# Optimization experiments

Measured on AMD Instinct MI355X. Metric: run time of the kernel, lower is better.

## Reference

```python
import jax, jax.numpy as jnp
import numpy as np

DIM = 512
HEADS = 8
DIM_HEAD = 64
INNER = HEADS * DIM_HEAD
SCALE = DIM_HEAD ** -0.5


def setup_inputs() -> dict:
    key = jax.random.key(0)
    ks = jax.random.split(key, 6)
    b, n = 2, 2048
    x = jax.random.normal(ks[0], (b, n, DIM), dtype=jnp.float32)
    # torch Linear(dim, 3*inner, bias=False): store as [in, out] for x @ W
    w_qkv = jax.random.normal(ks[1], (DIM, 3 * INNER), dtype=jnp.float32) * (DIM ** -0.5)
    # Conv2d(heads, heads, 1, bias=False) weights squeezed to [out_h, in_h]
    w_pre = jax.random.normal(ks[2], (HEADS, HEADS), dtype=jnp.float32) * (HEADS ** -0.5)
    w_post = jax.random.normal(ks[3], (HEADS, HEADS), dtype=jnp.float32) * (HEADS ** -0.5)
    w_out = jax.random.normal(ks[4], (INNER, DIM), dtype=jnp.float32) * (INNER ** -0.5)
    b_out = jax.random.normal(ks[5], (DIM,), dtype=jnp.float32) * 0.01
    return {"x": x, "w_qkv": w_qkv, "w_pre": w_pre, "w_post": w_post,
            "w_out": w_out, "b_out": b_out}


def reference(x, w_qkv, w_pre, w_post, w_out, b_out):
    b, n, _ = x.shape
    qkv = x @ w_qkv  # [b, n, 3*inner]
    q, k, v = jnp.split(qkv, 3, axis=-1)
    # b n (h d) -> b h n d
    split_heads = lambda t: t.reshape(b, n, HEADS, DIM_HEAD).transpose(0, 2, 1, 3)
    q, k, v = split_heads(q), split_heads(k), split_heads(v)
    dots = jnp.einsum('bhid,bhjd->bhij', q, k) * SCALE
    # pre-softmax talking-heads: 1x1 conv over the head axis
    dots = jnp.einsum('gh,bhij->bgij', w_pre, dots)
    attn = jax.nn.softmax(dots, axis=-1)
    # post-softmax talking-heads mix
    attn = jnp.einsum('gh,bhij->bgij', w_post, attn)
    out = jnp.einsum('bhij,bhjd->bhid', attn, v)
    out = out.transpose(0, 2, 1, 3).reshape(b, n, INNER)  # b h n d -> b n (h d)
    return out @ w_out + b_out
```

## Files before the change

### kernel.cpp

```cpp
#include <hip/hip_runtime.h>
#include <hip/hip_bf16.h>

typedef unsigned short ushort_t;
typedef __attribute__((ext_vector_type(8))) short short8;
typedef __attribute__((ext_vector_type(4))) short short4v;
typedef __attribute__((ext_vector_type(4))) float floatx4;

#define MFMA16(a, b, c) __builtin_amdgcn_mfma_f32_16x16x32_bf16(a, b, c, 0, 0, 0)

__device__ __forceinline__ float bf2f(ushort_t u) {
    unsigned int v = ((unsigned int)u) << 16;
    return __int_as_float((int)v);
}
__device__ __forceinline__ ushort_t f2bf(float f) {
    unsigned int x = (unsigned int)__float_as_int(f);
    unsigned int r = (x + 0x7FFFu + ((x >> 16) & 1u)) >> 16;
    return (ushort_t)r;
}

__global__ __launch_bounds__(256) void k_cvt(const floatx4* __restrict__ src,
                                             short4v* __restrict__ dst, int n4) {
    int i = blockIdx.x * 256 + threadIdx.x;
    if (i < n4) {
        floatx4 v = src[i];
        short4v o;
        o[0] = (short)f2bf(v[0]);
        o[1] = (short)f2bf(v[1]);
        o[2] = (short)f2bf(v[2]);
        o[3] = (short)f2bf(v[3]);
        dst[i] = o;
    }
}

__global__ __launch_bounds__(256) void k_transpose_cvt(const float* __restrict__ src,
                                                       ushort_t* __restrict__ dst, int R, int C) {
    __shared__ float t[32][33];
    int tx = threadIdx.x & 31, ty = threadIdx.x >> 5;
    int r0 = blockIdx.y * 32, c0 = blockIdx.x * 32;
    for (int y = ty; y < 32; y += 8) t[y][tx] = src[(r0 + y) * C + c0 + tx];
    __syncthreads();
    for (int y = ty; y < 32; y += 8) dst[(c0 + y) * R + r0 + tx] = f2bf(t[tx][y]);
}

__global__ __launch_bounds__(256) void k_qkv(const ushort_t* __restrict__ x,
                                             const ushort_t* __restrict__ wt,
                                             ushort_t* __restrict__ qs,
                                             ushort_t* __restrict__ ks,
                                             ushort_t* __restrict__ vt) {
    __shared__ __align__(16) ushort_t st[64 * 72];
    const int tid = threadIdx.x, lane = tid & 63, wv = tid >> 6;
    const int col = lane & 15, quad = lane >> 4;
    const int row0 = blockIdx.y * 64 + (wv >> 1) * 32;
    const int c0 = blockIdx.x * 64 + (wv & 1) * 32;
    const int which = blockIdx.x >> 3, hh = blockIdx.x & 7;
    const int brow0 = blockIdx.y * 64;
    const int bb = brow0 >> 11, n0 = brow0 & 2047;
    const int hidx = bb * 8 + hh;
    floatx4 acc[2][2];
#pragma unroll
    for (int i = 0; i < 2; i++)
#pragma unroll
        for (int j = 0; j < 2; j++) acc[i][j] = (floatx4){0.f, 0.f, 0.f, 0.f};
    for (int k0 = 0; k0 < 512; k0 += 32) {
        const int ko = k0 + quad * 8;
        short8 a0 = *(const short8*)&x[(row0 + col) * 512 + ko];
        short8 a1 = *(const short8*)&x[(row0 + 16 + col) * 512 + ko];
        short8 b0 = *(const short8*)&wt[(c0 + col) * 512 + ko];
        short8 b1 = *(const short8*)&wt[(c0 + 16 + col) * 512 + ko];
        acc[0][0] = MFMA16(a0, b0, acc[0][0]);
        acc[0][1] = MFMA16(a0, b1, acc[0][1]);
        acc[1][0] = MFMA16(a1, b0, acc[1][0]);
        acc[1][1] = MFMA16(a1, b1, acc[1][1]);
    }
    const float qscale = (which == 0) ? 0.125f : 1.0f;
#pragma unroll
    for (int i = 0; i < 2; i++)
#pragma unroll
        for (int j = 0; j < 2; j++)
#pragma unroll
            for (int r = 0; r < 4; r++) {
                int il = (wv >> 1) * 32 + i * 16 + quad * 4 + r;
                int cl = (wv & 1) * 32 + j * 16 + col;
                ushort_t hv = f2bf(acc[i][j][r] * qscale);
                if (which == 2) st[cl * 72 + il] = hv;
                else            st[il * 72 + cl] = hv;
            }
    __syncthreads();
    if (which < 2) {
        ushort_t* dst = (which == 0) ? qs : ks;
#pragma unroll
        for (int s = tid; s < 512; s += 256) {
            int rr = s >> 3, dc = (s & 7) * 8;
            *(short8*)&dst[(hidx * 2048 + n0 + rr) * 64 + dc] = *(const short8*)&st[rr * 72 + dc];
        }
    } else {
#pragma unroll
        for (int s = tid; s < 512; s += 256) {
            int d = s >> 3, nc = (s & 7) * 8;
            *(short8*)&vt[(hidx * 64 + d) * 2048 + n0 + nc] = *(const short8*)&st[d * 72 + nc];
        }
    }
}

__global__ __launch_bounds__(512, 2) void k_attn(const ushort_t* __restrict__ qs,
                                                 const ushort_t* __restrict__ ks,
                                                 const ushort_t* __restrict__ vt,
                                                 const float* __restrict__ w_pre,
                                                 const float* __restrict__ w_post,
                                                 const ushort_t* __restrict__ wot,
                                                 const float* __restrict__ bias,
                                                 float* __restrict__ out) {
    __shared__ __align__(16) ushort_t qlds[8 * 16 * 72];
    __shared__ __align__(16) ushort_t U[8 * 16 * 136];
    __shared__ __align__(16) ushort_t oline[16 * 520];
    __shared__ float wbuf[128];
    __shared__ float lred[8][8][16];
    __shared__ float linv[8][16];
    const int tid = threadIdx.x, lane = tid & 63, wv = tid >> 6;
    const int col = lane & 15, quad = lane >> 4;
    const int b = blockIdx.y, n0 = blockIdx.x * 16;
    const int e = wv;

    if (tid < 64) wbuf[tid] = w_pre[tid];
    else if (tid < 128) wbuf[tid] = w_post[tid - 64];
    for (int c = tid; c < 1024; c += 512) {
        int hh = c >> 7, rem = c & 127, ii = rem >> 3, dc = (rem & 7) * 8;
        *(short8*)&qlds[(hh * 16 + ii) * 72 + dc] =
            *(const short8*)&qs[((b * 8 + hh) * 2048 + n0 + ii) * 64 + dc];
    }
    __syncthreads();

    float Lacc[8][4];
    floatx4 Oa[8][4];
#pragma unroll
    for (int g = 0; g < 8; g++) {
#pragma unroll
        for (int r = 0; r < 4; r++) Lacc[g][r] = 0.f;
#pragma unroll
        for (int nt = 0; nt < 4; nt++) Oa[g][nt] = (floatx4){0.f, 0.f, 0.f, 0.f};
    }

    for (int jt = 0; jt < 16; jt++) {
        const int j0 = jt * 128;
        const int jw = j0 + wv * 16;
        floatx4 S[8];
#pragma unroll
        for (int h = 0; h < 8; h++) {
            const ushort_t* qb = &qlds[(h * 16 + col) * 72 + quad * 8];
            short8 a0 = *(const short8*)&qb[0];
            short8 a1 = *(const short8*)&qb[32];
            const ushort_t* kb = &ks[((b * 8 + h) * 2048 + jw + col) * 64 + quad * 8];
            short8 b0 = *(const short8*)&kb[0];
            short8 b1 = *(const short8*)&kb[32];
            floatx4 a = (floatx4){0.f, 0.f, 0.f, 0.f};
            a = MFMA16(a0, b0, a);
            a = MFMA16(a1, b1, a);
            S[h] = a;
        }
#pragma unroll
        for (int g = 0; g < 8; g++)
#pragma unroll
            for (int r = 0; r < 4; r++) {
                float s = 0.f;
#pragma unroll
                for (int h = 0; h < 8; h++) s = fmaf(wbuf[g * 8 + h], S[h][r], s);
                float u = __expf(s);
                Lacc[g][r] += u;
                U[(g * 16 + quad * 4 + r) * 136 + wv * 16 + col] = f2bf(u);
            }
        __syncthreads();
#pragma unroll
        for (int k2 = 0; k2 < 4; k2++) {
            short8 bf[4];
#pragma unroll
            for (int nt = 0; nt < 4; nt++)
                bf[nt] = *(const short8*)&vt[((b * 8 + e) * 64 + nt * 16 + col) * 2048 + j0 +
                                             k2 * 32 + quad * 8];
            short8 af[8];
#pragma unroll
            for (int g = 0; g < 8; g++)
                af[g] = *(const short8*)&U[(g * 16 + col) * 136 + k2 * 32 + quad * 8];
#pragma unroll
            for (int g = 0; g < 8; g++)
#pragma unroll
                for (int nt = 0; nt < 4; nt++) Oa[g][nt] = MFMA16(af[g], bf[nt], Oa[g][nt]);
        }
        __syncthreads();
    }

#pragma unroll
    for (int g = 0; g < 8; g++)
#pragma unroll
        for (int r = 0; r < 4; r++) {
            float v = Lacc[g][r];
            v += __shfl_xor(v, 1, 64);
            v += __shfl_xor(v, 2, 64);
            v += __shfl_xor(v, 4, 64);
            v += __shfl_xor(v, 8, 64);
            if (col == 0) lred[wv][g][quad * 4 + r] = v;
        }
    __syncthreads();
    if (tid < 128) {
        int g = tid >> 4, ii = tid & 15;
        float l = 0.f;
#pragma unroll
        for (int w2 = 0; w2 < 8; w2++) l += lred[w2][g][ii];
        linv[g][ii] = 1.0f / l;
    }
    __syncthreads();
    float coef[8][4];
#pragma unroll
    for (int g = 0; g < 8; g++) {
        float wqe = wbuf[64 + e * 8 + g];
#pragma unroll
        for (int r = 0; r < 4; r++) coef[g][r] = wqe * linv[g][quad * 4 + r];
    }
#pragma unroll
    for (int nt = 0; nt < 4; nt++)
#pragma unroll
        for (int r = 0; r < 4; r++) {
            float o = 0.f;
#pragma unroll
            for (int g = 0; g < 8; g++) o = fmaf(coef[g][r], Oa[g][nt][r], o);
            oline[(quad * 4 + r) * 520 + e * 64 + nt * 16 + col] = f2bf(o);
        }
    __syncthreads();
#pragma unroll
    for (int nt = 0; nt < 4; nt++) {
        floatx4 acc = (floatx4){0.f, 0.f, 0.f, 0.f};
        const int c = wv * 64 + nt * 16 + col;
#pragma unroll
        for (int k2 = 0; k2 < 16; k2++) {
            short8 af = *(const short8*)&oline[col * 520 + k2 * 32 + quad * 8];
            short8 bf = *(const short8*)&wot[c * 512 + k2 * 32 + quad * 8];
            acc = MFMA16(af, bf, acc);
        }
        float bz = bias[c];
#pragma unroll
        for (int r = 0; r < 4; r++)
            out[(b * 2048 + n0 + quad * 4 + r) * 512 + c] = acc[r] + bz;
    }
}

extern "C" void kernel_launch(void* const* d_in, const int* in_sizes, int n_in,
                              void* d_out, int out_size, void* d_ws, size_t ws_size,
                              hipStream_t stream) {
    const float* x = (const float*)d_in[0];
    const float* w_qkv = (const float*)d_in[1];
    const float* w_pre = (const float*)d_in[2];
    const float* w_post = (const float*)d_in[3];
    const float* w_out = (const float*)d_in[4];
    const float* b_out = (const float*)d_in[5];
    char* ws = (char*)d_ws;
    ushort_t* qs = (ushort_t*)(ws);
    ushort_t* ks = (ushort_t*)(ws + (4u << 20));
    ushort_t* vt = (ushort_t*)(ws + (8u << 20));
    ushort_t* xb = (ushort_t*)(ws + (12u << 20));
    ushort_t* wt = (ushort_t*)(ws + (16u << 20));
    ushort_t* wot = (ushort_t*)(ws + (16u << 20) + 1572864u);
    float* out = (float*)d_out;

    k_cvt<<<dim3(2048), dim3(256), 0, stream>>>((const floatx4*)x, (short4v*)xb, 524288);
    k_transpose_cvt<<<dim3(48, 16), dim3(256), 0, stream>>>(w_qkv, wt, 512, 1536);
    k_transpose_cvt<<<dim3(16, 16), dim3(256), 0, stream>>>(w_out, wot, 512, 512);
    k_qkv<<<dim3(24, 64), dim3(256), 0, stream>>>(xb, wt, qs, ks, vt);
    k_attn<<<dim3(128, 2), dim3(512), 0, stream>>>(qs, ks, vt, w_pre, w_post, wot, b_out, out);
}
```

Baseline: 308.3 us.

## Split softmax normalizers into a separate stats pass and mix post-heads before PV

Adds a k_stats kernel that computes the per-row softmax denominators for every mixed head, split across four key chunks, and writes partial sums to the workspace. The attention kernel then reads those sums, normalizes the probabilities on the fly and applies the post-softmax head mix before the PV product. Each wave therefore accumulates only its own output head, cutting the PV MFMAs and the accumulator registers by a factor of eight. The cost is a second full QK^T and exp pass, plus a post-mix of 64 FMAs per element inside the inner loop.

Result: slower. 379.6 us (+23.1%).

```diff
diff --git a/kernel.cpp b/kernel.cpp
--- a/kernel.cpp
+++ b/kernel.cpp
@@ -102,47 +102,28 @@
     }
 }
 
-__global__ __launch_bounds__(512, 2) void k_attn(const ushort_t* __restrict__ qs,
-                                                 const ushort_t* __restrict__ ks,
-                                                 const ushort_t* __restrict__ vt,
-                                                 const float* __restrict__ w_pre,
-                                                 const float* __restrict__ w_post,
-                                                 const ushort_t* __restrict__ wot,
-                                                 const float* __restrict__ bias,
-                                                 float* __restrict__ out) {
+__global__ __launch_bounds__(256, 4) void k_stats(const ushort_t* __restrict__ qs,
+                                                  const ushort_t* __restrict__ ks,
+                                                  const float* __restrict__ w_pre,
+                                                  float* __restrict__ lpart) {
     __shared__ __align__(16) ushort_t qlds[8 * 16 * 72];
-    __shared__ __align__(16) ushort_t U[8 * 16 * 136];
-    __shared__ __align__(16) ushort_t oline[16 * 520];
-    __shared__ float wbuf[128];
-    __shared__ float lred[8][8][16];
-    __shared__ float linv[8][16];
+    __shared__ float lred[4][8][16];
     const int tid = threadIdx.x, lane = tid & 63, wv = tid >> 6;
     const int col = lane & 15, quad = lane >> 4;
-    const int b = blockIdx.y, n0 = blockIdx.x * 16;
-    const int e = wv;
-
-    if (tid < 64) wbuf[tid] = w_pre[tid];
-    else if (tid < 128) wbuf[tid] = w_post[tid - 64];
-    for (int c = tid; c < 1024; c += 512) {
+    const int jc = blockIdx.x, b = blockIdx.z, n0 = blockIdx.y * 16;
+    for (int c = tid; c < 1024; c += 256) {
         int hh = c >> 7, rem = c & 127, ii = rem >> 3, dc = (rem & 7) * 8;
         *(short8*)&qlds[(hh * 16 + ii) * 72 + dc] =
             *(const short8*)&qs[((b * 8 + hh) * 2048 + n0 + ii) * 64 + dc];
     }
     __syncthreads();
-
     float Lacc[8][4];
-    floatx4 Oa[8][4];
-#pragma unroll
-    for (int g = 0; g < 8; g++) {
+#pragma unroll
+    for (int g = 0; g < 8; g++)
 #pragma unroll
         for (int r = 0; r < 4; r++) Lacc[g][r] = 0.f;
-#pragma unroll
-        for (int nt = 0; nt < 4; nt++) Oa[g][nt] = (floatx4){0.f, 0.f, 0.f, 0.f};
-    }
-
-    for (int jt = 0; jt < 16; jt++) {
-        const int j0 = jt * 128;
-        const int jw = j0 + wv * 16;
+    for (int it = 0; it < 8; it++) {
+        const int jw = jc * 512 + it * 64 + wv * 16;
         floatx4 S[8];
 #pragma unroll
         for (int h = 0; h < 8; h++) {
@@ -163,31 +144,10 @@
             for (int r = 0; r < 4; r++) {
                 float s = 0.f;
 #pragma unroll
-                for (int h = 0; h < 8; h++) s = fmaf(wbuf[g * 8 + h], S[h][r], s);
-                float u = __expf(s);
-                Lacc[g][r] += u;
-                U[(g * 16 + quad * 4 + r) * 136 + wv * 16 + col] = f2bf(u);
-            }
-        __syncthreads();
-#pragma unroll
-        for (int k2 = 0; k2 < 4; k2++) {
-            short8 bf[4];
-#pragma unroll
-            for (int nt = 0; nt < 4; nt++)
-                bf[nt] = *(const short8*)&vt[((b * 8 + e) * 64 + nt * 16 + col) * 2048 + j0 +
-                                             k2 * 32 + quad * 8];
-            short8 af[8];
-#pragma unroll
-            for (int g = 0; g < 8; g++)
-                af[g] = *(const short8*)&U[(g * 16 + col) * 136 + k2 * 32 + quad * 8];
-#pragma unroll
-            for (int g = 0; g < 8; g++)
-#pragma unroll
-                for (int nt = 0; nt < 4; nt++) Oa[g][nt] = MFMA16(af[g], bf[nt], Oa[g][nt]);
-        }
-        __syncthreads();
-    }
-
+                for (int h = 0; h < 8; h++) s = fmaf(w_pre[g * 8 + h], S[h][r], s);
+                Lacc[g][r] += __expf(s);
+            }
+    }
 #pragma unroll
     for (int g = 0; g < 8; g++)
 #pragma unroll
@@ -202,28 +162,108 @@
     __syncthreads();
     if (tid < 128) {
         int g = tid >> 4, ii = tid & 15;
+        float l = lred[0][g][ii] + lred[1][g][ii] + lred[2][g][ii] + lred[3][g][ii];
+        lpart[((b * 4 + jc) * 8 + g) * 2048 + n0 + ii] = l;
+    }
+}
+
+__global__ __launch_bounds__(512, 2) void k_attn(const ushort_t* __restrict__ qs,
+                                                 const ushort_t* __restrict__ ks,
+                                                 const ushort_t* __restrict__ vt,
+                                                 const float* __restrict__ w_pre,
+                                                 const float* __restrict__ w_post,
+                                                 const float* __restrict__ lpart,
+                                                 const ushort_t* __restrict__ wot,
+                                                 const float* __restrict__ bias,
+                                                 float* __restrict__ out) {
+    __shared__ __align__(16) ushort_t qlds[8 * 16 * 72];
+    __shared__ __align__(16) ushort_t amix[8 * 16 * 136];
+    __shared__ __align__(16) ushort_t oline[16 * 520];
+    __shared__ float linv[8][16];
+    const int tid = threadIdx.x, lane = tid & 63, wv = tid >> 6;
+    const int col = lane & 15, quad = lane >> 4;
+    const int b = blockIdx.y, n0 = blockIdx.x * 16;
+    const int e = wv;
+
+    for (int c = tid; c < 1024; c += 512) {
+        int hh = c >> 7, rem = c & 127, ii = rem >> 3, dc = (rem & 7) * 8;
+        *(short8*)&qlds[(hh * 16 + ii) * 72 + dc] =
+            *(const short8*)&qs[((b * 8 + hh) * 2048 + n0 + ii) * 64 + dc];
+    }
+    if (tid < 128) {
+        int g = tid >> 4, ii = tid & 15;
         float l = 0.f;
 #pragma unroll
-        for (int w2 = 0; w2 < 8; w2++) l += lred[w2][g][ii];
+        for (int jc = 0; jc < 4; jc++) l += lpart[((b * 4 + jc) * 8 + g) * 2048 + n0 + ii];
         linv[g][ii] = 1.0f / l;
     }
     __syncthreads();
-    float coef[8][4];
-#pragma unroll
-    for (int g = 0; g < 8; g++) {
-        float wqe = wbuf[64 + e * 8 + g];
-#pragma unroll
-        for (int r = 0; r < 4; r++) coef[g][r] = wqe * linv[g][quad * 4 + r];
+    float lr[8][4];
+#pragma unroll
+    for (int g = 0; g < 8; g++)
+#pragma unroll
+        for (int r = 0; r < 4; r++) lr[g][r] = linv[g][quad * 4 + r];
+
+    floatx4 O[4];
+#pragma unroll
+    for (int nt = 0; nt < 4; nt++) O[nt] = (floatx4){0.f, 0.f, 0.f, 0.f};
+
+    for (int jt = 0; jt < 16; jt++) {
+        const int j0 = jt * 128;
+        const int jw = j0 + wv * 16;
+        floatx4 S[8];
+#pragma unroll
+        for (int h = 0; h < 8; h++) {
+            const ushort_t* qb = &qlds[(h * 16 + col) * 72 + quad * 8];
+            short8 a0 = *(const short8*)&qb[0];
+            short8 a1 = *(const short8*)&qb[32];
+            const ushort_t* kb = &ks[((b * 8 + h) * 2048 + jw + col) * 64 + quad * 8];
+            short8 b0 = *(const short8*)&kb[0];
+            short8 b1 = *(const short8*)&kb[32];
+            floatx4 a = (floatx4){0.f, 0.f, 0.f, 0.f};
+            a = MFMA16(a0, b0, a);
+            a = MFMA16(a1, b1, a);
+            S[h] = a;
+        }
+        float P[8][4];
+#pragma unroll
+        for (int g = 0; g < 8; g++)
+#pragma unroll
+            for (int r = 0; r < 4; r++) {
+                float s = 0.f;
+#pragma unroll
+                for (int h = 0; h < 8; h++) s = fmaf(w_pre[g * 8 + h], S[h][r], s);
+                P[g][r] = __expf(s) * lr[g][r];
+            }
+#pragma unroll
+        for (int e2 = 0; e2 < 8; e2++)
+#pragma unroll
+            for (int r = 0; r < 4; r++) {
+                float a = 0.f;
+#pragma unroll
+                for (int g = 0; g < 8; g++) a = fmaf(w_post[e2 * 8 + g], P[g][r], a);
+                amix[(e2 * 16 + quad * 4 + r) * 136 + wv * 16 + col] = f2bf(a);
+            }
+        __syncthreads();
+#pragma unroll
+        for (int nt = 0; nt < 4; nt++) {
+            floatx4 a = O[nt];
+#pragma unroll
+            for (int k2 = 0; k2 < 4; k2++) {
+                short8 af = *(const short8*)&amix[(e * 16 + col) * 136 + k2 * 32 + quad * 8];
+                short8 bf = *(const short8*)&vt[((b * 8 + e) * 64 + nt * 16 + col) * 2048 + j0 +
+                                                k2 * 32 + quad * 8];
+                a = MFMA16(af, bf, a);
+            }
+            O[nt] = a;
+        }
+        __syncthreads();
     }
 #pragma unroll
     for (int nt = 0; nt < 4; nt++)
 #pragma unroll
-        for (int r = 0; r < 4; r++) {
-            float o = 0.f;
-#pragma unroll
-            for (int g = 0; g < 8; g++) o = fmaf(coef[g][r], Oa[g][nt][r], o);
-            oline[(quad * 4 + r) * 520 + e * 64 + nt * 16 + col] = f2bf(o);
-        }
+        for (int r = 0; r < 4; r++)
+            oline[(quad * 4 + r) * 520 + e * 64 + nt * 16 + col] = f2bf(O[nt][r]);
     __syncthreads();
 #pragma unroll
     for (int nt = 0; nt < 4; nt++) {
@@ -258,11 +298,13 @@
     ushort_t* xb = (ushort_t*)(ws + (12u << 20));
     ushort_t* wt = (ushort_t*)(ws + (16u << 20));
     ushort_t* wot = (ushort_t*)(ws + (16u << 20) + 1572864u);
+    float* lpart = (float*)(ws + (18u << 20));
     float* out = (float*)d_out;
 
     k_cvt<<<dim3(2048), dim3(256), 0, stream>>>((const floatx4*)x, (short4v*)xb, 524288);
     k_transpose_cvt<<<dim3(48, 16), dim3(256), 0, stream>>>(w_qkv, wt, 512, 1536);
     k_transpose_cvt<<<dim3(16, 16), dim3(256), 0, stream>>>(w_out, wot, 512, 512);
     k_qkv<<<dim3(24, 64), dim3(256), 0, stream>>>(xb, wt, qs, ks, vt);
-    k_attn<<<dim3(128, 2), dim3(512), 0, stream>>>(qs, ks, vt, w_pre, w_post, wot, b_out, out);
-}
+    k_stats<<<dim3(4, 128, 2), dim3(256), 0, stream>>>(qs, ks, w_pre, lpart);
+    k_attn<<<dim3(128, 2), dim3(512), 0, stream>>>(qs, ks, vt, w_pre, w_post, lpart, wot, b_out, out);
+}
```

## Enlarge QKV GEMM tile, packed-FMA head mixing, and share attention LDS buffers

Applied to the files above, without the earlier changes.

The QKV projection kernel now computes a 128x64 tile per block, with each wave covering 32x64 instead of 32x32. This doubles B-operand reuse and halves the grid. The attention kernel moves from launch_bounds(512,2) to (512,1), giving the compiler more registers. It reads the talking-heads weights directly from global memory instead of an LDS copy and uses packed float2 FMAs for the pre-softmax mix. It pads U rows to 140, reuses U as the output staging buffer to cut LDS use, and loads A fragments one at a time. The risks are lower occupancy in the attention kernel and fewer QKV blocks to spread across CUs.

New measurement: 321.3 us. 4.2% more time.

```diff
diff --git a/kernel.cpp b/kernel.cpp
--- a/kernel.cpp
+++ b/kernel.cpp
@@ -5,6 +5,7 @@
 typedef __attribute__((ext_vector_type(8))) short short8;
 typedef __attribute__((ext_vector_type(4))) short short4v;
 typedef __attribute__((ext_vector_type(4))) float floatx4;
+typedef __attribute__((ext_vector_type(2))) float floatx2;
 
 #define MFMA16(a, b, c) __builtin_amdgcn_mfma_f32_16x16x32_bf16(a, b, c, 0, 0, 0)
 
@@ -42,67 +43,73 @@
     for (int y = ty; y < 32; y += 8) dst[(c0 + y) * R + r0 + tx] = f2bf(t[tx][y]);
 }
 
-__global__ __launch_bounds__(256) void k_qkv(const ushort_t* __restrict__ x,
-                                             const ushort_t* __restrict__ wt,
-                                             ushort_t* __restrict__ qs,
-                                             ushort_t* __restrict__ ks,
-                                             ushort_t* __restrict__ vt) {
-    __shared__ __align__(16) ushort_t st[64 * 72];
+__global__ __launch_bounds__(256, 3) void k_qkv(const ushort_t* __restrict__ x,
+                                                const ushort_t* __restrict__ wt,
+                                                ushort_t* __restrict__ qs,
+                                                ushort_t* __restrict__ ks,
+                                                ushort_t* __restrict__ vt) {
+    __shared__ __align__(16) ushort_t st[9216];
     const int tid = threadIdx.x, lane = tid & 63, wv = tid >> 6;
     const int col = lane & 15, quad = lane >> 4;
-    const int row0 = blockIdx.y * 64 + (wv >> 1) * 32;
-    const int c0 = blockIdx.x * 64 + (wv & 1) * 32;
     const int which = blockIdx.x >> 3, hh = blockIdx.x & 7;
-    const int brow0 = blockIdx.y * 64;
-    const int bb = brow0 >> 11, n0 = brow0 & 2047;
+    const int c0 = blockIdx.x * 64;
+    const int absrow0 = blockIdx.y * 128;
+    const int bb = blockIdx.y >> 4, n0 = (blockIdx.y & 15) * 128;
     const int hidx = bb * 8 + hh;
-    floatx4 acc[2][2];
+    const int row0 = absrow0 + wv * 32;
+    floatx4 acc[2][4];
 #pragma unroll
     for (int i = 0; i < 2; i++)
 #pragma unroll
-        for (int j = 0; j < 2; j++) acc[i][j] = (floatx4){0.f, 0.f, 0.f, 0.f};
+        for (int j = 0; j < 4; j++) acc[i][j] = (floatx4){0.f, 0.f, 0.f, 0.f};
     for (int k0 = 0; k0 < 512; k0 += 32) {
         const int ko = k0 + quad * 8;
         short8 a0 = *(const short8*)&x[(row0 + col) * 512 + ko];
         short8 a1 = *(const short8*)&x[(row0 + 16 + col) * 512 + ko];
         short8 b0 = *(const short8*)&wt[(c0 + col) * 512 + ko];
         short8 b1 = *(const short8*)&wt[(c0 + 16 + col) * 512 + ko];
+        short8 b2 = *(const short8*)&wt[(c0 + 32 + col) * 512 + ko];
+        short8 b3 = *(const short8*)&wt[(c0 + 48 + col) * 512 + ko];
         acc[0][0] = MFMA16(a0, b0, acc[0][0]);
         acc[0][1] = MFMA16(a0, b1, acc[0][1]);
+        acc[0][2] = MFMA16(a0, b2, acc[0][2]);
+        acc[0][3] = MFMA16(a0, b3, acc[0][3]);
         acc[1][0] = MFMA16(a1, b0, acc[1][0]);
         acc[1][1] = MFMA16(a1, b1, acc[1][1]);
+        acc[1][2] = MFMA16(a1, b2, acc[1][2]);
+        acc[1][3] = MFMA16(a1, b3, acc[1][3]);
     }
     const float qscale = (which == 0) ? 0.125f : 1.0f;
 #pragma unroll
     for (int i = 0; i < 2; i++)
 #pragma unroll
-        for (int j = 0; j < 2; j++)
+        for (int j = 0; j < 4; j++)
 #pragma unroll
             for (int r = 0; r < 4; r++) {
-                int il = (wv >> 1) * 32 + i * 16 + quad * 4 + r;
-                int cl = (wv & 1) * 32 + j * 16 + col;
+                int il = wv * 32 + i * 16 + quad * 4 + r;
+                int cl = j * 16 + col;
                 ushort_t hv = f2bf(acc[i][j][r] * qscale);
-                if (which == 2) st[cl * 72 + il] = hv;
+                if (which == 2) st[cl * 136 + il] = hv;
                 else            st[il * 72 + cl] = hv;
             }
     __syncthreads();
     if (which < 2) {
         ushort_t* dst = (which == 0) ? qs : ks;
 #pragma unroll
-        for (int s = tid; s < 512; s += 256) {
+        for (int s = tid; s < 1024; s += 256) {
             int rr = s >> 3, dc = (s & 7) * 8;
             *(short8*)&dst[(hidx * 2048 + n0 + rr) * 64 + dc] = *(const short8*)&st[rr * 72 + dc];
         }
     } else {
 #pragma unroll
-        for (int s = tid; s < 512; s += 256) {
-            int d = s >> 3, nc = (s & 7) * 8;
-            *(short8*)&vt[(hidx * 64 + d) * 2048 + n0 + nc] = *(const short8*)&st[d * 72 + nc];
-        }
-    }
-}
-
-__global__ __launch_bounds__(512, 2) void k_attn(const ushort_t* __restrict__ qs,
+        for (int s = tid; s < 1024; s += 256) {
+            int d = s >> 4, nc = (s & 15) * 8;
+            *(short8*)&vt[(hidx * 64 + d) * 2048 + n0 + nc] = *(const short8*)&st[d * 136 + nc];
+        }
+    }
+}
+
+__global__ __launch_bounds__(512, 1) void k_attn(const ushort_t* __restrict__ qs,
                                                  const ushort_t* __restrict__ ks,
                                                  const ushort_t* __restrict__ vt,
                                                  const float* __restrict__ w_pre,
@@ -111,9 +118,7 @@
                                                  const float* __restrict__ bias,
                                                  float* __restrict__ out) {
     __shared__ __align__(16) ushort_t qlds[8 * 16 * 72];
-    __shared__ __align__(16) ushort_t U[8 * 16 * 136];
-    __shared__ __align__(16) ushort_t oline[16 * 520];
-    __shared__ float wbuf[128];
+    __shared__ __align__(16) ushort_t U[8 * 16 * 140];
     __shared__ float lred[8][8][16];
     __shared__ float linv[8][16];
     const int tid = threadIdx.x, lane = tid & 63, wv = tid >> 6;
@@ -121,8 +126,6 @@
     const int b = blockIdx.y, n0 = blockIdx.x * 16;
     const int e = wv;
 
-    if (tid < 64) wbuf[tid] = w_pre[tid];
-    else if (tid < 128) wbuf[tid] = w_post[tid - 64];
     for (int c = tid; c < 1024; c += 512) {
         int hh = c >> 7, rem = c & 127, ii = rem >> 3, dc = (rem & 7) * 8;
         *(short8*)&qlds[(hh * 16 + ii) * 72 + dc] =
@@ -130,18 +133,18 @@
     }
     __syncthreads();
 
+    floatx4 Oa[8][4];
     float Lacc[8][4];
-    floatx4 Oa[8][4];
 #pragma unroll
     for (int g = 0; g < 8; g++) {
 #pragma unroll
+        for (int nt = 0; nt < 4; nt++) Oa[g][nt] = (floatx4){0.f, 0.f, 0.f, 0.f};
+#pragma unroll
         for (int r = 0; r < 4; r++) Lacc[g][r] = 0.f;
-#pragma unroll
-        for (int nt = 0; nt < 4; nt++) Oa[g][nt] = (floatx4){0.f, 0.f, 0.f, 0.f};
-    }
-
-    for (int jt = 0; jt < 16; jt++) {
-        const int j0 = jt * 128;
+    }
+
+    for (int tile = 0; tile < 16; tile++) {
+        const int j0 = tile * 128;
         const int jw = j0 + wv * 16;
         floatx4 S[8];
 #pragma unroll
@@ -160,13 +163,18 @@
 #pragma unroll
         for (int g = 0; g < 8; g++)
 #pragma unroll
-            for (int r = 0; r < 4; r++) {
-                float s = 0.f;
-#pragma unroll
-                for (int h = 0; h < 8; h++) s = fmaf(wbuf[g * 8 + h], S[h][r], s);
-                float u = __expf(s);
-                Lacc[g][r] += u;
-                U[(g * 16 + quad * 4 + r) * 136 + wv * 16 + col] = f2bf(u);
+            for (int r2 = 0; r2 < 2; r2++) {
+                floatx2 s = (floatx2){0.f, 0.f};
+#pragma unroll
+                for (int h = 0; h < 8; h++) {
+                    floatx2 sv = (floatx2){S[h][2 * r2], S[h][2 * r2 + 1]};
+                    s += sv * w_pre[g * 8 + h];
+                }
+                float u0 = __expf(s.x), u1 = __expf(s.y);
+                Lacc[g][2 * r2] += u0;
+                Lacc[g][2 * r2 + 1] += u1;
+                U[(g * 16 + quad * 4 + 2 * r2) * 140 + wv * 16 + col] = f2bf(u0);
+                U[(g * 16 + quad * 4 + 2 * r2 + 1) * 140 + wv * 16 + col] = f2bf(u1);
             }
         __syncthreads();
 #pragma unroll
@@ -176,14 +184,12 @@
             for (int nt = 0; nt < 4; nt++)
                 bf[nt] = *(const short8*)&vt[((b * 8 + e) * 64 + nt * 16 + col) * 2048 + j0 +
                                              k2 * 32 + quad * 8];
-            short8 af[8];
-#pragma unroll
-            for (int g = 0; g < 8; g++)
-                af[g] = *(const short8*)&U[(g * 16 + col) * 136 + k2 * 32 + quad * 8];
-#pragma unroll
-            for (int g = 0; g < 8; g++)
-#pragma unroll
-                for (int nt = 0; nt < 4; nt++) Oa[g][nt] = MFMA16(af[g], bf[nt], Oa[g][nt]);
+#pragma unroll
+            for (int g = 0; g < 8; g++) {
+                short8 af = *(const short8*)&U[(g * 16 + col) * 140 + k2 * 32 + quad * 8];
+#pragma unroll
+                for (int nt = 0; nt < 4; nt++) Oa[g][nt] = MFMA16(af, bf[nt], Oa[g][nt]);
+            }
         }
         __syncthreads();
     }
@@ -211,10 +217,11 @@
     float coef[8][4];
 #pragma unroll
     for (int g = 0; g < 8; g++) {
-        float wqe = wbuf[64 + e * 8 + g];
+        float wqe = w_post[e * 8 + g];
 #pragma unroll
         for (int r = 0; r < 4; r++) coef[g][r] = wqe * linv[g][quad * 4 + r];
     }
+    ushort_t* oline = U;
 #pragma unroll
     for (int nt = 0; nt < 4; nt++)
 #pragma unroll
@@ -263,6 +270,6 @@
     k_cvt<<<dim3(2048), dim3(256), 0, stream>>>((const floatx4*)x, (short4v*)xb, 524288);
     k_transpose_cvt<<<dim3(48, 16), dim3(256), 0, stream>>>(w_qkv, wt, 512, 1536);
     k_transpose_cvt<<<dim3(16, 16), dim3(256), 0, stream>>>(w_out, wot, 512, 512);
-    k_qkv<<<dim3(24, 64), dim3(256), 0, stream>>>(xb, wt, qs, ks, vt);
+    k_qkv<<<dim3(24, 32), dim3(256), 0, stream>>>(xb, wt, qs, ks, vt);
     k_attn<<<dim3(128, 2), dim3(512), 0, stream>>>(qs, ks, vt, w_pre, w_post, wot, b_out, out);
 }
```
